# Kernel tuning notes

Hardware: AMD Instinct MI355X
Metric: run time of the kernel (lower is better)

Reference implementation:

```python
import jax, jax.numpy as jnp
import numpy as np
from jax import lax

B, T, D_IN, D_OUT = 8, 4096, 256, 256


def setup_inputs() -> dict:
    key = jax.random.key(0)
    k1, k2, k3, k4, k5 = jax.random.split(key, 5)
    bound_in = 1.0 / np.sqrt(D_IN)
    return {
        "inputs": jax.random.normal(k1, (B, T, D_IN), dtype=jnp.float32),
        "mask": jnp.zeros((B, T, 1), dtype=jnp.float32),
        "W_in": jax.random.uniform(k2, (D_OUT, D_IN), jnp.float32, -bound_in, bound_in),
        "b_in": jax.random.uniform(k3, (D_OUT,), jnp.float32, -bound_in, bound_in),
        "W_f": jax.random.uniform(k4, (D_OUT, D_IN), jnp.float32, -bound_in, bound_in),
        "b_f": jax.random.uniform(k5, (D_OUT,), jnp.float32, -bound_in, bound_in),
    }


def _forget_mult(f, x):
    # h_t = f_t * x_t + (1 - f_t) * h_{t-1}, h_{-1} = 0 (torchqrnn ForgetMult, hidden_init=None)
    fT = jnp.swapaxes(f, 0, 1)  # (T, B, D)
    xT = jnp.swapaxes(x, 0, 1)

    def step(h, fx):
        ft, xt = fx
        h = ft * xt + (1.0 - ft) * h
        return h, h

    h0 = jnp.zeros(xT.shape[1:], dtype=x.dtype)  # (B, D)
    _, hs = lax.scan(step, h0, (fT, xT))
    return jnp.swapaxes(hs, 0, 1)  # (B, T, D)


def reference(inputs, mask, W_in, b_in, W_f, b_f):
    # right_to_left = False -> no flips
    x = jnp.tanh(jnp.einsum("btd,od->bto", inputs, W_in) + b_in)
    f = jax.nn.sigmoid(jnp.einsum("btd,od->bto", inputs, W_f) + b_f + mask * 10000.0)
    return _forget_mult(f, x)
```

## Files before the change

kernel.cpp:

```cpp
#include <hip/hip_runtime.h>
#include <math.h>


typedef _Float16 f16x8 __attribute__((ext_vector_type(8)));
typedef float f32x4 __attribute__((ext_vector_type(4)));
typedef float f32x16 __attribute__((ext_vector_type(16)));
typedef unsigned int u32x4 __attribute__((ext_vector_type(4)));

constexpr int B_ = 8, T_ = 4096, D_ = 256, K_ = 256;
constexpr int M_ = B_ * T_;
constexpr int CHUNK = 32;
constexpr int NCH = T_ / CHUNK;
constexpr int NBLK = M_ / CHUNK;
constexpr int SLICE_EL = 8192;

struct alignas(4) XF { _Float16 x, f; };
struct alignas(4) HP2 { _Float16 h, p; };
union UHP { unsigned int u; HP2 hp; XF xf; };

__device__ __forceinline__ float fexp2(float a) { return __builtin_amdgcn_exp2f(a); }
__device__ __forceinline__ float frcp(float a) { return __builtin_amdgcn_rcpf(a); }
constexpr float L2E = 1.4426950408889634f;

__device__ __forceinline__ float fast_sigmoid(float z) {
  return frcp(1.f + fexp2(-z * L2E));
}
__device__ __forceinline__ float fast_tanh(float z) {
  const float t = fexp2(-2.f * L2E * fabsf(z));
  return copysignf((1.f - t) * frcp(1.f + t), z);
}

__global__ __launch_bounds__(256) void wconv(const float* __restrict__ Win,
                                             const float* __restrict__ Wf,
                                             _Float16* __restrict__ Wh2) {
  const int t = blockIdx.x * 256 + threadIdx.x;
  const int n = t & 255;
  const int kc = (t >> 8) & 1;
  const int mat = (t >> 9) & 1;
  const int kk2 = t >> 10;
  const float* s = (mat ? Wf : Win) + (size_t)n * K_ + kk2 * 16 + kc * 8;
  f32x4 a = *(const f32x4*)s;
  f32x4 b = *(const f32x4*)(s + 4);
  f16x8 o;
  o[0] = (_Float16)a[0]; o[1] = (_Float16)a[1];
  o[2] = (_Float16)a[2]; o[3] = (_Float16)a[3];
  o[4] = (_Float16)b[0]; o[5] = (_Float16)b[1];
  o[6] = (_Float16)b[2]; o[7] = (_Float16)b[3];
  *(f16x8*)(Wh2 + (size_t)t * 8) = o;
}

__global__ __launch_bounds__(256, 4) void gemm_hp(
    const float* __restrict__ A, const _Float16* __restrict__ Wh2,
    const float* __restrict__ bin, const float* __restrict__ bfv,
    const float* __restrict__ mask, unsigned int* __restrict__ HPout,
    float* __restrict__ Ap, float* __restrict__ Hp) {
  __shared__ __align__(16) char smem[32768];
  char* ldsA = smem;

  const int tid = threadIdx.x;
  const int w = tid >> 6, lane = tid & 63;
  const int nl = lane & 31, kh = lane >> 5;
  const int g = blockIdx.x;
  const int row0 = g * CHUNK;

  f32x16 acc[2][2];
#pragma unroll
  for (int mat = 0; mat < 2; ++mat)
#pragma unroll
    for (int nt = 0; nt < 2; ++nt) acc[mat][nt] = (f32x16)(0.f);

  {
    const int am = tid >> 3;
    const int ak4 = (tid & 7) * 4;
    const float* agp = A + (size_t)(row0 + am) * K_ + (tid & 7) * 32;
#pragma unroll
    for (int j = 0; j < 4; ++j) {
      const int kcg = ak4 + j;
      f32x4 lo = *(const f32x4*)(agp + j * 8);
      f32x4 hi = *(const f32x4*)(agp + j * 8 + 4);
      f16x8 t;
      t[0] = (_Float16)lo[0]; t[1] = (_Float16)lo[1];
      t[2] = (_Float16)lo[2]; t[3] = (_Float16)lo[3];
      t[4] = (_Float16)hi[0]; t[5] = (_Float16)hi[1];
      t[6] = (_Float16)hi[2]; t[7] = (_Float16)hi[3];
      *(f16x8*)(ldsA + am * 512 + ((kcg ^ am) << 4)) = t;
    }
  }
  __syncthreads();

  {
    const _Float16* wfrag = Wh2 + (size_t)(kh * 256 + w * 64 + nl) * 8;
    for (int kk2 = 0; kk2 < 16; ++kk2) {
      f16x8 afr;
      {
        const int kcg = kk2 * 2 + kh;
        afr = *(const f16x8*)(ldsA + nl * 512 + ((kcg ^ nl) << 4));
      }
#pragma unroll
      for (int mat = 0; mat < 2; ++mat)
#pragma unroll
        for (int nt = 0; nt < 2; ++nt) {
          f16x8 bfr = *(const f16x8*)(wfrag + (size_t)(mat * 512 + nt * 32) * 8);
          acc[mat][nt] = __builtin_amdgcn_mfma_f32_32x32x16_f16(
              afr, bfr, acc[mat][nt], 0, 0, 0);
        }
      wfrag += SLICE_EL;
    }
  }
  __syncthreads();

  float bx[2], bf[2];
#pragma unroll
  for (int nt = 0; nt < 2; ++nt) {
    const int col = w * 64 + nt * 32 + nl;
    bx[nt] = bin[col];
    bf[nt] = bfv[col];
  }
  float madd[16];
#pragma unroll
  for (int reg = 0; reg < 16; ++reg) {
    const int rl = (reg & 3) + 8 * (reg >> 2) + 4 * kh;
    madd[reg] = 10000.f * mask[row0 + rl];
  }

#pragma unroll
  for (int nt = 0; nt < 2; ++nt) {
    const int col = w * 64 + nt * 32 + nl;
#pragma unroll
    for (int reg = 0; reg < 16; ++reg) {
      const int rloc = (reg & 3) + 8 * (reg >> 2) + 4 * kh;
      const float zx = acc[0][nt][reg] + bx[nt];
      const float zf = acc[1][nt][reg] + bf[nt] + madd[reg];
      XF v;
      v.x = (_Float16)fast_tanh(zx);
      v.f = (_Float16)fast_sigmoid(zf);
      *(XF*)(smem + ((size_t)rloc * D_ + col) * 4) = v;
    }
  }
  __syncthreads();

  const int d = tid;
  float hrun = 0.f, Prun = 1.f;
#pragma unroll 8
  for (int t = 0; t < 32; ++t) {
    char* slot = smem + ((size_t)t * D_ + d) * 4;
    const XF v = *(const XF*)slot;
    const float f = (float)v.f;
    const float a = 1.f - f;
    hrun = f * (float)v.x + a * hrun;
    Prun *= a;
    HP2 o;
    o.h = (_Float16)hrun;
    o.p = (_Float16)Prun;
    *(HP2*)slot = o;
  }
  __syncthreads();

#pragma unroll
  for (int j = 0; j < 8; ++j) {
    const int c = j * 256 + tid;
    u32x4 vv = *(const u32x4*)(smem + (size_t)c * 16);
    *(u32x4*)(HPout + (size_t)g * 8192 + (size_t)c * 4) = vv;
  }

  Ap[(size_t)g * D_ + d] = Prun;
  Hp[(size_t)g * D_ + d] = hrun;
}

__global__ __launch_bounds__(256) void scan_mid(const float* __restrict__ Ap,
                                                const float* __restrict__ Hp,
                                                float* __restrict__ hs) {
  const int b = blockIdx.x, d = threadIdx.x;
  float h = 0.f;
#pragma unroll 8
  for (int c = 0; c < NCH; ++c) {
    const size_t i = ((size_t)(b * NCH + c)) * D_ + d;
    hs[i] = h;
    h = Hp[i] + Ap[i] * h;
  }
}

__global__ __launch_bounds__(256) void final_k(const unsigned int* __restrict__ HP,
                                               const float* __restrict__ hs,
                                               float* __restrict__ out) {
  const int g = blockIdx.x;
  const int wv = threadIdx.x >> 6;
  const int d0 = (threadIdx.x & 63) * 4;
  const f32x4 h0 = *(const f32x4*)(hs + (size_t)g * D_ + d0);
#pragma unroll 4
  for (int tt = 0; tt < 8; ++tt) {
    const int t = wv * 8 + tt;
    const size_t idx = ((size_t)g * CHUNK + t) * D_ + d0;
    u32x4 u = *(const u32x4*)(HP + idx);
    f32x4 o;
#pragma unroll
    for (int i = 0; i < 4; ++i) {
      UHP q; q.u = u[i];
      o[i] = (float)q.hp.h + (float)q.hp.p * h0[i];
    }
    *(f32x4*)(out + idx) = o;
  }
}

extern "C" void kernel_launch(void* const* d_in, const int* in_sizes, int n_in,
                              void* d_out, int out_size, void* d_ws, size_t ws_size,
                              hipStream_t stream) {
  const float* inputs = (const float*)d_in[0];
  const float* mask   = (const float*)d_in[1];
  const float* W_in   = (const float*)d_in[2];
  const float* b_in   = (const float*)d_in[3];
  const float* W_f    = (const float*)d_in[4];
  const float* b_f    = (const float*)d_in[5];
  float* out = (float*)d_out;
  char* ws = (char*)d_ws;

  constexpr size_t HPSZ = (size_t)M_ * D_ * 4;
  constexpr size_t WSZ  = (size_t)2 * 256 * 256 * 2;
  constexpr size_t SUM  = (size_t)NBLK * D_ * sizeof(float);

  unsigned int* HPb = (unsigned int*)ws;
  _Float16* Wh2 = (_Float16*)(ws + HPSZ);
  float* Ap = (float*)(ws + HPSZ + WSZ);
  float* Hp = (float*)(ws + HPSZ + WSZ + SUM);
  float* hs = (float*)(ws + HPSZ + WSZ + 2 * SUM);

  wconv<<<64, 256, 0, stream>>>(W_in, W_f, Wh2);
  gemm_hp<<<NBLK, 256, 0, stream>>>(inputs, Wh2, b_in, b_f, mask, HPb, Ap, Hp);
  scan_mid<<<B_, 256, 0, stream>>>(Ap, Hp, hs);
  final_k<<<NBLK, 256, 0, stream>>>(HPb, hs, out);
}
```

Baseline: 127.2 us.

## Split GEMM block into 8 waves, one weight matrix per wave group

Doubles the gemm_hp block from 256 to 512 threads so waves 0-3 compute the tanh (x) projection and waves 4-7 the sigmoid (forget) projection, each wave holding two accumulators instead of four. The A-tile load and the HP writeback are spread over twice as many threads, and only the first 256 threads run the per-chunk sequential scan. The aim is more waves per CU and more latency hiding during the MFMA and activation phases, with fewer registers per thread. In exchange, half the threads sit idle during the scan phase, and each x/f half is written to LDS separately.

```diff
diff --git a/kernel.cpp b/kernel.cpp
--- a/kernel.cpp
+++ b/kernel.cpp
@@ -49,7 +49,7 @@
   *(f16x8*)(Wh2 + (size_t)t * 8) = o;
 }
 
-__global__ __launch_bounds__(256, 4) void gemm_hp(
+__global__ __launch_bounds__(512, 6) void gemm_hp(
     const float* __restrict__ A, const _Float16* __restrict__ Wh2,
     const float* __restrict__ bin, const float* __restrict__ bfv,
     const float* __restrict__ mask, unsigned int* __restrict__ HPout,
@@ -60,22 +60,20 @@
   const int tid = threadIdx.x;
   const int w = tid >> 6, lane = tid & 63;
   const int nl = lane & 31, kh = lane >> 5;
+  const int mat = w >> 2, cg = w & 3;
   const int g = blockIdx.x;
   const int row0 = g * CHUNK;
 
-  f32x16 acc[2][2];
-#pragma unroll
-  for (int mat = 0; mat < 2; ++mat)
-#pragma unroll
-    for (int nt = 0; nt < 2; ++nt) acc[mat][nt] = (f32x16)(0.f);
+  f32x16 acc[2];
+  acc[0] = (f32x16)(0.f);
+  acc[1] = (f32x16)(0.f);
 
   {
-    const int am = tid >> 3;
-    const int ak4 = (tid & 7) * 4;
-    const float* agp = A + (size_t)(row0 + am) * K_ + (tid & 7) * 32;
-#pragma unroll
-    for (int j = 0; j < 4; ++j) {
-      const int kcg = ak4 + j;
+    const int am = tid >> 4;
+    const float* agp = A + (size_t)(row0 + am) * K_ + (tid & 15) * 16;
+#pragma unroll
+    for (int j = 0; j < 2; ++j) {
+      const int kcg = (tid & 15) * 2 + j;
       f32x4 lo = *(const f32x4*)(agp + j * 8);
       f32x4 hi = *(const f32x4*)(agp + j * 8 + 4);
       f16x8 t;
@@ -89,82 +87,88 @@
   __syncthreads();
 
   {
-    const _Float16* wfrag = Wh2 + (size_t)(kh * 256 + w * 64 + nl) * 8;
+    const _Float16* wfrag =
+        Wh2 + (size_t)((mat * 2 + kh) * 256 + cg * 64 + nl) * 8;
     for (int kk2 = 0; kk2 < 16; ++kk2) {
       f16x8 afr;
       {
         const int kcg = kk2 * 2 + kh;
         afr = *(const f16x8*)(ldsA + nl * 512 + ((kcg ^ nl) << 4));
       }
-#pragma unroll
-      for (int mat = 0; mat < 2; ++mat)
-#pragma unroll
-        for (int nt = 0; nt < 2; ++nt) {
-          f16x8 bfr = *(const f16x8*)(wfrag + (size_t)(mat * 512 + nt * 32) * 8);
-          acc[mat][nt] = __builtin_amdgcn_mfma_f32_32x32x16_f16(
-              afr, bfr, acc[mat][nt], 0, 0, 0);
-        }
+      f16x8 b0 = *(const f16x8*)(wfrag);
+      f16x8 b1 = *(const f16x8*)(wfrag + 32 * 8);
+      acc[0] = __builtin_amdgcn_mfma_f32_32x32x16_f16(afr, b0, acc[0], 0, 0, 0);
+      acc[1] = __builtin_amdgcn_mfma_f32_32x32x16_f16(afr, b1, acc[1], 0, 0, 0);
       wfrag += SLICE_EL;
     }
   }
   __syncthreads();
 
-  float bx[2], bf[2];
-#pragma unroll
-  for (int nt = 0; nt < 2; ++nt) {
-    const int col = w * 64 + nt * 32 + nl;
-    bx[nt] = bin[col];
-    bf[nt] = bfv[col];
-  }
-  float madd[16];
-#pragma unroll
-  for (int reg = 0; reg < 16; ++reg) {
-    const int rl = (reg & 3) + 8 * (reg >> 2) + 4 * kh;
-    madd[reg] = 10000.f * mask[row0 + rl];
-  }
-
-#pragma unroll
-  for (int nt = 0; nt < 2; ++nt) {
-    const int col = w * 64 + nt * 32 + nl;
+  if (mat == 0) {
+    const float b0 = bin[cg * 64 + nl], b1 = bin[cg * 64 + 32 + nl];
+#pragma unroll
+    for (int nt = 0; nt < 2; ++nt) {
+      const int col = cg * 64 + nt * 32 + nl;
+#pragma unroll
+      for (int reg = 0; reg < 16; ++reg) {
+        const int rloc = (reg & 3) + 8 * (reg >> 2) + 4 * kh;
+        const float zx = acc[nt][reg] + (nt ? b1 : b0);
+        *(_Float16*)(smem + ((size_t)rloc * D_ + col) * 4) =
+            (_Float16)fast_tanh(zx);
+      }
+    }
+  } else {
+    const float b0 = bfv[cg * 64 + nl], b1 = bfv[cg * 64 + 32 + nl];
+    float madd[16];
 #pragma unroll
     for (int reg = 0; reg < 16; ++reg) {
-      const int rloc = (reg & 3) + 8 * (reg >> 2) + 4 * kh;
-      const float zx = acc[0][nt][reg] + bx[nt];
-      const float zf = acc[1][nt][reg] + bf[nt] + madd[reg];
-      XF v;
-      v.x = (_Float16)fast_tanh(zx);
-      v.f = (_Float16)fast_sigmoid(zf);
-      *(XF*)(smem + ((size_t)rloc * D_ + col) * 4) = v;
-    }
-  }
-  __syncthreads();
-
-  const int d = tid;
+      const int rl = (reg & 3) + 8 * (reg >> 2) + 4 * kh;
+      madd[reg] = 10000.f * mask[row0 + rl];
+    }
+#pragma unroll
+    for (int nt = 0; nt < 2; ++nt) {
+      const int col = cg * 64 + nt * 32 + nl;
+#pragma unroll
+      for (int reg = 0; reg < 16; ++reg) {
+        const int rloc = (reg & 3) + 8 * (reg >> 2) + 4 * kh;
+        const float zf = acc[nt][reg] + (nt ? b1 : b0) + madd[reg];
+        *(_Float16*)(smem + ((size_t)rloc * D_ + col) * 4 + 2) =
+            (_Float16)fast_sigmoid(zf);
+      }
+    }
+  }
+  __syncthreads();
+
   float hrun = 0.f, Prun = 1.f;
+  if (tid < D_) {
+    const int d = tid;
 #pragma unroll 8
-  for (int t = 0; t < 32; ++t) {
-    char* slot = smem + ((size_t)t * D_ + d) * 4;
-    const XF v = *(const XF*)slot;
-    const float f = (float)v.f;
-    const float a = 1.f - f;
-    hrun = f * (float)v.x + a * hrun;
-    Prun *= a;
-    HP2 o;
-    o.h = (_Float16)hrun;
-    o.p = (_Float16)Prun;
-    *(HP2*)slot = o;
-  }
-  __syncthreads();
-
-#pragma unroll
-  for (int j = 0; j < 8; ++j) {
-    const int c = j * 256 + tid;
+    for (int t = 0; t < 32; ++t) {
+      char* slot = smem + ((size_t)t * D_ + d) * 4;
+      const XF v = *(const XF*)slot;
+      const float f = (float)v.f;
+      const float a = 1.f - f;
+      hrun = f * (float)v.x + a * hrun;
+      Prun *= a;
+      HP2 o;
+      o.h = (_Float16)hrun;
+      o.p = (_Float16)Prun;
+      *(HP2*)slot = o;
+    }
+  }
+  __syncthreads();
+
+#pragma unroll
+  for (int j = 0; j < 4; ++j) {
+    const int c = j * 512 + tid;
     u32x4 vv = *(const u32x4*)(smem + (size_t)c * 16);
     *(u32x4*)(HPout + (size_t)g * 8192 + (size_t)c * 4) = vv;
   }
 
-  Ap[(size_t)g * D_ + d] = Prun;
-  Hp[(size_t)g * D_ + d] = hrun;
+  if (tid < D_) {
+    Ap[(size_t)g * D_ + tid] = Prun;
+    Hp[(size_t)g * D_ + tid] = hrun;
+  }
 }
 
 __global__ __launch_bounds__(256) void scan_mid(const float* __restrict__ Ap,
@@ -225,7 +229,7 @@
   float* hs = (float*)(ws + HPSZ + WSZ + 2 * SUM);
 
   wconv<<<64, 256, 0, stream>>>(W_in, W_f, Wh2);
-  gemm_hp<<<NBLK, 256, 0, stream>>>(inputs, Wh2, b_in, b_f, mask, HPb, Ap, Hp);
+  gemm_hp<<<NBLK, 512, 0, stream>>>(inputs, Wh2, b_in, b_f, mask, HPb, Ap, Hp);
   scan_mid<<<B_, 256, 0, stream>>>(Ap, Hp, hs);
   final_k<<<NBLK, 256, 0, stream>>>(HPb, hs, out);
 }
```

Result: faster. 124.7 us (-2.0%).
